# Kernel tuning notes

Measured on AMD Instinct MI355X. Metric: run time of the kernel, lower is better.

Reference implementation:

```python
import jax, jax.numpy as jnp
import numpy as np
from math import sqrt

N = 8192
INPUT_SIZE = 256
D_MODEL = 256


def setup_inputs() -> dict:
    key = jax.random.key(0)
    k1, k2, k3, k4 = jax.random.split(key, 4)
    x = jax.random.normal(k1, (N, INPUT_SIZE), dtype=jnp.float32)
    adj = jax.random.randint(k2, (N, N), 0, 2, dtype=jnp.int32)
    # torch nn.Linear(input_size, d_model): weight [d_model, input_size], bias [d_model]
    bound = 1.0 / sqrt(INPUT_SIZE)
    Vw = jax.random.uniform(k3, (D_MODEL, INPUT_SIZE), dtype=jnp.float32, minval=-bound, maxval=bound)
    Vb = jax.random.uniform(k4, (D_MODEL,), dtype=jnp.float32, minval=-bound, maxval=bound)
    return {"x": x, "adj": adj, "Vw": Vw, "Vb": Vb}


def reference(x, adj, Vw, Vb):
    # value = V(x)
    value = x @ Vw.T + Vb                                  # [N, d_model]
    # scores = x x^T / sqrt(d_model), masked where adj == 0
    scores = (x @ x.T) * (1.0 / sqrt(D_MODEL))             # [N, N]
    scores = jnp.where(adj == 0, jnp.float32(-1e9), scores)
    p_attn = jax.nn.softmax(scores, axis=-1)               # [N, N]
    Vs = p_attn @ value                                    # [N, d_model]
    return (Vs, p_attn)
```

## Files before the change

### kernel.cpp

```cpp
#include <hip/hip_runtime.h>
#include <hip/hip_bf16.h>


#define NN 8192
#define DD 256

typedef __attribute__((ext_vector_type(8))) short bf16x8;
typedef __attribute__((ext_vector_type(8))) unsigned short u16x8;
typedef __attribute__((ext_vector_type(4))) float f32x4;

__device__ __forceinline__ unsigned short f2bf(float f) {
  unsigned u = __builtin_bit_cast(unsigned, f);
  u += 0x7fffu + ((u >> 16) & 1u);
  return (unsigned short)(u >> 16);
}
__device__ __forceinline__ float bf2f(unsigned short h) {
  unsigned u = ((unsigned)h) << 16;
  return __builtin_bit_cast(float, u);
}
__device__ __forceinline__ unsigned pack2(float a, float b) {
  return (unsigned)f2bf(a) | ((unsigned)f2bf(b) << 16);
}

__global__ void k_prep_x(const float* __restrict__ x, unsigned short* __restrict__ xb) {
  int t = blockIdx.x * 256 + threadIdx.x;
  const float4* s = reinterpret_cast<const float4*>(x) + (size_t)t * 2;
  float4 f0 = s[0], f1 = s[1];
  uint4 o;
  o.x = pack2(f0.x, f0.y); o.y = pack2(f0.z, f0.w);
  o.z = pack2(f1.x, f1.y); o.w = pack2(f1.z, f1.w);
  reinterpret_cast<uint4*>(xb)[t] = o;
}

__global__ __launch_bounds__(256) void k_value(
    const float* __restrict__ Vw, const float* __restrict__ Vb,
    const unsigned short* __restrict__ xb, unsigned short* __restrict__ vT) {
  __shared__ unsigned short lB[64 * 256];
  int mb = blockIdx.x >> 2, nb = blockIdx.x & 3;
  int tid = threadIdx.x, lane = tid & 63, w = tid >> 6;
  int mw = w >> 1, nw = w & 1;
  {
    int n_l = tid >> 2, q = tid & 3;
#pragma unroll
    for (int o = 0; o < 8; ++o) {
      int k0 = q * 64 + o * 8;
      const float4* src = reinterpret_cast<const float4*>(Vw + (nb * 64 + n_l) * DD + k0);
      float4 g0 = src[0], g1 = src[1];
      uint4 pk;
      pk.x = pack2(g0.x, g0.y); pk.y = pack2(g0.z, g0.w);
      pk.z = pack2(g1.x, g1.y); pk.w = pack2(g1.z, g1.w);
      *reinterpret_cast<uint4*>(reinterpret_cast<char*>(lB) + n_l * 512 + ((k0 * 2) ^ ((n_l & 7) << 4))) = pk;
    }
  }
  bf16x8 aR[2][8];
#pragma unroll
  for (int mf = 0; mf < 2; ++mf) {
    int rg = mb * 64 + mw * 32 + mf * 16 + (lane & 15);
    const char* base = reinterpret_cast<const char*>(xb + (size_t)rg * DD);
#pragma unroll
    for (int ks = 0; ks < 8; ++ks)
      aR[mf][ks] = *reinterpret_cast<const bf16x8*>(base + ks * 64 + ((lane >> 4) * 16));
  }
  __syncthreads();
  f32x4 acc[2][2] = {};
#pragma unroll
  for (int ks = 0; ks < 8; ++ks) {
    int kb = ks * 64 + ((lane >> 4) * 16);
#pragma unroll
    for (int nf = 0; nf < 2; ++nf) {
      int n = nw * 32 + nf * 16 + (lane & 15);
      bf16x8 b = *reinterpret_cast<const bf16x8*>(reinterpret_cast<const char*>(lB) + n * 512 + (kb ^ ((n & 7) << 4)));
#pragma unroll
      for (int mf = 0; mf < 2; ++mf)
        acc[mf][nf] = __builtin_amdgcn_mfma_f32_16x16x32_bf16(aR[mf][ks], b, acc[mf][nf], 0, 0, 0);
    }
  }
#pragma unroll
  for (int nf = 0; nf < 2; ++nf) {
    int n_g = nb * 64 + nw * 32 + nf * 16 + (lane & 15);
    float vb = Vb[n_g];
#pragma unroll
    for (int mf = 0; mf < 2; ++mf) {
      int m_g = mb * 64 + mw * 32 + mf * 16 + ((lane >> 4) << 2);
      ushort4 h;
      h.x = f2bf(acc[mf][nf][0] + vb);
      h.y = f2bf(acc[mf][nf][1] + vb);
      h.z = f2bf(acc[mf][nf][2] + vb);
      h.w = f2bf(acc[mf][nf][3] + vb);
      *reinterpret_cast<ushort4*>(vT + (size_t)n_g * NN + m_g) = h;
    }
  }
}

__global__ __launch_bounds__(256) void k_pass1(
    const unsigned short* __restrict__ xb, const int* __restrict__ adj,
    unsigned short* __restrict__ ews, float* __restrict__ lpart) {
  __shared__ char smem[65536];
  int rb = blockIdx.x >> 6, cb = blockIdx.x & 63;
  int tid = threadIdx.x, lane = tid & 63, w = tid >> 6;
  int mw = w >> 1, wc = w & 1;
#pragma unroll
  for (int c = 0; c < 16; ++c) {
    int id = c * 256 + tid;
    int col = id >> 5, oct = id & 31;
    uint4 v = *reinterpret_cast<const uint4*>(xb + (size_t)(cb * 128 + col) * DD + oct * 8);
    *reinterpret_cast<uint4*>(smem + col * 512 + ((oct * 16) ^ ((col & 7) << 4))) = v;
  }
  bf16x8 aR[2][8];
#pragma unroll
  for (int mf = 0; mf < 2; ++mf) {
    int rg = rb * 64 + mw * 32 + mf * 16 + (lane & 15);
    const char* base = reinterpret_cast<const char*>(xb + (size_t)rg * DD);
#pragma unroll
    for (int ks = 0; ks < 8; ++ks)
      aR[mf][ks] = *reinterpret_cast<const bf16x8*>(base + ks * 64 + ((lane >> 4) * 16));
  }
  __syncthreads();
  int r0 = rb * 64 + mw * 32 + ((lane >> 4) << 2);
  int c0 = cb * 128 + wc * 64 + (lane & 15);
  int aj[2][4][4];
#pragma unroll
  for (int mf = 0; mf < 2; ++mf)
#pragma unroll
    for (int nf = 0; nf < 4; ++nf)
#pragma unroll
      for (int i = 0; i < 4; ++i)
        aj[mf][nf][i] = __builtin_nontemporal_load(adj + (size_t)(r0 + mf * 16 + i) * NN + (c0 + nf * 16));
  f32x4 acc[2][4] = {};
#pragma unroll
  for (int ks = 0; ks < 8; ++ks) {
    int kb = ks * 64 + ((lane >> 4) * 16);
#pragma unroll
    for (int nf = 0; nf < 4; ++nf) {
      int cc = wc * 64 + nf * 16 + (lane & 15);
      bf16x8 b = *reinterpret_cast<const bf16x8*>(smem + cc * 512 + (kb ^ ((cc & 7) << 4)));
#pragma unroll
      for (int mf = 0; mf < 2; ++mf)
        acc[mf][nf] = __builtin_amdgcn_mfma_f32_16x16x32_bf16(aR[mf][ks], b, acc[mf][nf], 0, 0, 0);
    }
  }
#pragma unroll
  for (int mf = 0; mf < 2; ++mf)
#pragma unroll
    for (int nf = 0; nf < 4; ++nf)
#pragma unroll
      for (int i = 0; i < 4; ++i) {
        float e = aj[mf][nf][i] ? __expf(acc[mf][nf][i] * 0.0625f) : 0.f;
        unsigned short h = f2bf(e);
        ews[(size_t)(r0 + mf * 16 + i) * NN + (c0 + nf * 16)] = h;
        acc[mf][nf][i] = bf2f(h);
      }
  __syncthreads();
  float* ls = reinterpret_cast<float*>(smem);
#pragma unroll
  for (int mf = 0; mf < 2; ++mf)
#pragma unroll
    for (int i = 0; i < 4; ++i) {
      float r = acc[mf][0][i] + acc[mf][1][i] + acc[mf][2][i] + acc[mf][3][i];
      r += __shfl_xor(r, 1); r += __shfl_xor(r, 2);
      r += __shfl_xor(r, 4); r += __shfl_xor(r, 8);
      if ((lane & 15) == 0)
        ls[wc * 64 + mw * 32 + mf * 16 + ((lane >> 4) << 2) + i] = r;
    }
  __syncthreads();
  if (tid < 64)
    lpart[(size_t)cb * NN + rb * 64 + tid] = ls[tid] + ls[64 + tid];
}

__global__ void k_reduce_l(const float* __restrict__ lpart, float* __restrict__ rl) {
  int i = blockIdx.x * 256 + threadIdx.x;
  float s = 0.f;
  for (int c = 0; c < 64; ++c) s += lpart[(size_t)c * NN + i];
  rl[i] = s > 0.f ? 1.f / s : 0.f;
}

__global__ __launch_bounds__(512) void k_vs(
    const unsigned short* __restrict__ ews, const unsigned short* __restrict__ vT,
    const float* __restrict__ rl, unsigned short* __restrict__ vspb) {
  __shared__ char lV[2][65536];
  int rt = blockIdx.x >> 2, ck = blockIdx.x & 3;
  int tid = threadIdx.x, lane = tid & 63, w = tid >> 6;
  int ln = lane & 15, kq = lane >> 4;
  int row = rt * 128 + w * 16 + ln;
  const unsigned short* ap = ews + (size_t)row * NN + ck * 2048 + kq * 8;

#define LOADB(G, KC)                                                                     \
  _Pragma("unroll") for (int q = 0; q < 8; ++q) {                                        \
    int id_ = q * 512 + tid, n_ = id_ >> 4, o_ = id_ & 15;                               \
    (G)[q] = *reinterpret_cast<const uint4*>(vT + (size_t)n_ * NN + ck * 2048 + (KC) * 128 + o_ * 8); \
  }
#define DSWRITE(G, BB)                                                                   \
  _Pragma("unroll") for (int q = 0; q < 8; ++q) {                                        \
    int id_ = q * 512 + tid, n_ = id_ >> 4, o_ = id_ & 15;                               \
    *reinterpret_cast<uint4*>(&lV[BB][n_ * 256 + ((o_ * 16) ^ ((n_ & 7) << 4))]) = (G)[q]; \
  }
#define LOADA(A, KC)                                                                     \
  _Pragma("unroll") for (int s_ = 0; s_ < 4; ++s_)                                       \
    (A)[s_] = *reinterpret_cast<const bf16x8*>(ap + (KC) * 128 + s_ * 32);

  uint4 gB[8];
  bf16x8 aC[4], aN[4];
  LOADB(gB, 0);
  LOADA(aC, 0);
  DSWRITE(gB, 0);
  __syncthreads();

  f32x4 acc[16] = {};
  for (int kc = 0; kc < 16; ++kc) {
    bool has = kc < 15;
    if (has) {
      LOADB(gB, kc + 1);
      LOADA(aN, kc + 1);
    }
    const char* bufc = lV[kc & 1];
#pragma unroll
    for (int ks = 0; ks < 4; ++ks) {
#pragma unroll
      for (int nf = 0; nf < 16; ++nf) {
        int n = nf * 16 + ln;
        bf16x8 b = *reinterpret_cast<const bf16x8*>(bufc + n * 256 + ((ks * 64 + kq * 16) ^ ((n & 7) << 4)));
        acc[nf] = __builtin_amdgcn_mfma_f32_16x16x32_bf16(aC[ks], b, acc[nf], 0, 0, 0);
      }
    }
    if (has) DSWRITE(gB, (kc + 1) & 1);
    __syncthreads();
#pragma unroll
    for (int s = 0; s < 4; ++s) aC[s] = aN[s];
  }

  int rowo = rt * 128 + w * 16 + kq * 4;
#pragma unroll
  for (int i = 0; i < 4; ++i) {
    float rli = rl[rowo + i];
#pragma unroll
    for (int nf = 0; nf < 16; ++nf) {
      int n = nf * 16 + ln;
      vspb[((size_t)ck * NN + rowo + i) * DD + n] = f2bf(acc[nf][i] * rli);
    }
  }
#undef LOADB
#undef DSWRITE
#undef LOADA
}

__global__ void k_norm(const unsigned short* __restrict__ ews, const float* __restrict__ rl,
                       float* __restrict__ pout) {
  size_t t = (size_t)blockIdx.x * 256 + threadIdx.x;
  float r = rl[t >> 10];
  u16x8 v = *reinterpret_cast<const u16x8*>(ews + t * 8);
  f32x4 o0, o1;
  o0[0] = bf2f(v[0]) * r; o0[1] = bf2f(v[1]) * r; o0[2] = bf2f(v[2]) * r; o0[3] = bf2f(v[3]) * r;
  o1[0] = bf2f(v[4]) * r; o1[1] = bf2f(v[5]) * r; o1[2] = bf2f(v[6]) * r; o1[3] = bf2f(v[7]) * r;
  f32x4* pd = reinterpret_cast<f32x4*>(pout + t * 8);
  __builtin_nontemporal_store(o0, pd);
  __builtin_nontemporal_store(o1, pd + 1);
}

__global__ void k_reduce_vs(const unsigned short* __restrict__ vspb, float* __restrict__ vout) {
  int t = blockIdx.x * 256 + threadIdx.x;
  float s[8] = {};
#pragma unroll
  for (int c = 0; c < 4; ++c) {
    u16x8 v = *reinterpret_cast<const u16x8*>(vspb + (size_t)c * NN * DD + (size_t)t * 8);
#pragma unroll
    for (int j = 0; j < 8; ++j) s[j] += bf2f(v[j]);
  }
  float4 o0, o1;
  o0.x = s[0]; o0.y = s[1]; o0.z = s[2]; o0.w = s[3];
  o1.x = s[4]; o1.y = s[5]; o1.z = s[6]; o1.w = s[7];
  float4* d = reinterpret_cast<float4*>(vout + (size_t)t * 8);
  d[0] = o0; d[1] = o1;
}

extern "C" void kernel_launch(void* const* d_in, const int* in_sizes, int n_in,
                              void* d_out, int out_size, void* d_ws, size_t ws_size,
                              hipStream_t stream) {
  const float* x   = (const float*)d_in[0];
  const int*   adj = (const int*)d_in[1];
  const float* Vw  = (const float*)d_in[2];
  const float* Vb  = (const float*)d_in[3];
  float* out   = (float*)d_out;
  float* vs_out = out;
  float* p_out  = out + (size_t)NN * DD;
  char* ws = (char*)d_ws;
  unsigned short* xb   = (unsigned short*)(ws);
  unsigned short* vT   = (unsigned short*)(ws + ((size_t)4  << 20));
  float* lpart         = (float*)(ws + ((size_t)8  << 20));
  float* rl            = (float*)(ws + ((size_t)10 << 20));
  unsigned short* vspb = (unsigned short*)(ws + ((size_t)11 << 20));
  unsigned short* ews  = (unsigned short*)(ws + ((size_t)27 << 20));

  k_prep_x<<<dim3(1024), dim3(256), 0, stream>>>(x, xb);
  k_value<<<dim3(512), dim3(256), 0, stream>>>(Vw, Vb, xb, vT);
  k_pass1<<<dim3(8192), dim3(256), 0, stream>>>(xb, adj, ews, lpart);
  k_reduce_l<<<dim3(32), dim3(256), 0, stream>>>(lpart, rl);
  k_vs<<<dim3(256), dim3(512), 0, stream>>>(ews, vT, rl, vspb);
  k_norm<<<dim3(32768), dim3(256), 0, stream>>>(ews, rl, p_out);
  k_reduce_vs<<<dim3(1024), dim3(256), 0, stream>>>(vspb, vs_out);
}
```

Measured before the change: 325.8 us.

## Pack adjacency mask into bits in a separate pass and add nontemporal loads

Adds a prepass that reads the int32 adjacency matrix with coalesced nontemporal vector loads and packs it into a bitmask. k_pass1 then reads one 64-bit mask word per row instead of scattered strided int32 loads. The nontemporal ews loads in k_vs and k_norm are meant to keep these streams from polluting cache. The same 256MB of adj is still read once, so the gain rests on better coalescing in pass1, at the cost of an extra kernel launch and an 8MB write.

```diff
diff --git a/kernel.cpp b/kernel.cpp
--- a/kernel.cpp
+++ b/kernel.cpp
@@ -8,6 +8,7 @@
 typedef __attribute__((ext_vector_type(8))) short bf16x8;
 typedef __attribute__((ext_vector_type(8))) unsigned short u16x8;
 typedef __attribute__((ext_vector_type(4))) float f32x4;
+typedef __attribute__((ext_vector_type(4))) int i32x4;
 
 __device__ __forceinline__ unsigned short f2bf(float f) {
   unsigned u = __builtin_bit_cast(unsigned, f);
@@ -30,6 +31,19 @@
   o.x = pack2(f0.x, f0.y); o.y = pack2(f0.z, f0.w);
   o.z = pack2(f1.x, f1.y); o.w = pack2(f1.z, f1.w);
   reinterpret_cast<uint4*>(xb)[t] = o;
+}
+
+__global__ void k_prep_adj(const int* __restrict__ adj, unsigned char* __restrict__ adjp) {
+  size_t t = (size_t)blockIdx.x * 256 + threadIdx.x;
+  const i32x4* s = reinterpret_cast<const i32x4*>(adj) + t * 2;
+  i32x4 v0 = __builtin_nontemporal_load(s);
+  i32x4 v1 = __builtin_nontemporal_load(s + 1);
+  unsigned b = 0;
+  b |= (v0[0] != 0) ? 1u : 0u;  b |= (v0[1] != 0) ? 2u : 0u;
+  b |= (v0[2] != 0) ? 4u : 0u;  b |= (v0[3] != 0) ? 8u : 0u;
+  b |= (v1[0] != 0) ? 16u : 0u; b |= (v1[1] != 0) ? 32u : 0u;
+  b |= (v1[2] != 0) ? 64u : 0u; b |= (v1[3] != 0) ? 128u : 0u;
+  adjp[t] = (unsigned char)b;
 }
 
 __global__ __launch_bounds__(256) void k_value(
@@ -93,12 +107,13 @@
 }
 
 __global__ __launch_bounds__(256) void k_pass1(
-    const unsigned short* __restrict__ xb, const int* __restrict__ adj,
+    const unsigned short* __restrict__ xb, const unsigned long long* __restrict__ adjp,
     unsigned short* __restrict__ ews, float* __restrict__ lpart) {
   __shared__ char smem[65536];
   int rb = blockIdx.x >> 6, cb = blockIdx.x & 63;
   int tid = threadIdx.x, lane = tid & 63, w = tid >> 6;
   int mw = w >> 1, wc = w & 1;
+  int ln = lane & 15, kq = lane >> 4;
 #pragma unroll
   for (int c = 0; c < 16; ++c) {
     int id = c * 256 + tid;
@@ -109,43 +124,42 @@
   bf16x8 aR[2][8];
 #pragma unroll
   for (int mf = 0; mf < 2; ++mf) {
-    int rg = rb * 64 + mw * 32 + mf * 16 + (lane & 15);
+    int rg = rb * 64 + mw * 32 + mf * 16 + ln;
     const char* base = reinterpret_cast<const char*>(xb + (size_t)rg * DD);
 #pragma unroll
     for (int ks = 0; ks < 8; ++ks)
-      aR[mf][ks] = *reinterpret_cast<const bf16x8*>(base + ks * 64 + ((lane >> 4) * 16));
-  }
-  __syncthreads();
-  int r0 = rb * 64 + mw * 32 + ((lane >> 4) << 2);
-  int c0 = cb * 128 + wc * 64 + (lane & 15);
-  int aj[2][4][4];
+      aR[mf][ks] = *reinterpret_cast<const bf16x8*>(base + ks * 64 + kq * 16);
+  }
+  __syncthreads();
+  int r0 = rb * 64 + mw * 32 + (kq << 2);
+  unsigned long long mrow[2][4];
 #pragma unroll
   for (int mf = 0; mf < 2; ++mf)
 #pragma unroll
-    for (int nf = 0; nf < 4; ++nf)
-#pragma unroll
-      for (int i = 0; i < 4; ++i)
-        aj[mf][nf][i] = __builtin_nontemporal_load(adj + (size_t)(r0 + mf * 16 + i) * NN + (c0 + nf * 16));
+    for (int i = 0; i < 4; ++i)
+      mrow[mf][i] = adjp[(size_t)(r0 + mf * 16 + i) * 128 + cb * 2 + wc];
   f32x4 acc[2][4] = {};
 #pragma unroll
   for (int ks = 0; ks < 8; ++ks) {
-    int kb = ks * 64 + ((lane >> 4) * 16);
+    int kb = ks * 64 + kq * 16;
 #pragma unroll
     for (int nf = 0; nf < 4; ++nf) {
-      int cc = wc * 64 + nf * 16 + (lane & 15);
+      int cc = wc * 64 + nf * 16 + ln;
       bf16x8 b = *reinterpret_cast<const bf16x8*>(smem + cc * 512 + (kb ^ ((cc & 7) << 4)));
 #pragma unroll
       for (int mf = 0; mf < 2; ++mf)
         acc[mf][nf] = __builtin_amdgcn_mfma_f32_16x16x32_bf16(aR[mf][ks], b, acc[mf][nf], 0, 0, 0);
     }
   }
+  int c0 = cb * 128 + wc * 64 + ln;
 #pragma unroll
   for (int mf = 0; mf < 2; ++mf)
 #pragma unroll
     for (int nf = 0; nf < 4; ++nf)
 #pragma unroll
       for (int i = 0; i < 4; ++i) {
-        float e = aj[mf][nf][i] ? __expf(acc[mf][nf][i] * 0.0625f) : 0.f;
+        bool on = (mrow[mf][i] >> (nf * 16 + ln)) & 1;
+        float e = on ? __expf(acc[mf][nf][i] * 0.0625f) : 0.f;
         unsigned short h = f2bf(e);
         ews[(size_t)(r0 + mf * 16 + i) * NN + (c0 + nf * 16)] = h;
         acc[mf][nf][i] = bf2f(h);
@@ -159,8 +173,8 @@
       float r = acc[mf][0][i] + acc[mf][1][i] + acc[mf][2][i] + acc[mf][3][i];
       r += __shfl_xor(r, 1); r += __shfl_xor(r, 2);
       r += __shfl_xor(r, 4); r += __shfl_xor(r, 8);
-      if ((lane & 15) == 0)
-        ls[wc * 64 + mw * 32 + mf * 16 + ((lane >> 4) << 2) + i] = r;
+      if (ln == 0)
+        ls[wc * 64 + mw * 32 + mf * 16 + (kq << 2) + i] = r;
     }
   __syncthreads();
   if (tid < 64)
@@ -196,7 +210,7 @@
   }
 #define LOADA(A, KC)                                                                     \
   _Pragma("unroll") for (int s_ = 0; s_ < 4; ++s_)                                       \
-    (A)[s_] = *reinterpret_cast<const bf16x8*>(ap + (KC) * 128 + s_ * 32);
+    (A)[s_] = __builtin_nontemporal_load(reinterpret_cast<const bf16x8*>(ap + (KC) * 128 + s_ * 32));
 
   uint4 gB[8];
   bf16x8 aC[4], aN[4];
@@ -247,7 +261,7 @@
                        float* __restrict__ pout) {
   size_t t = (size_t)blockIdx.x * 256 + threadIdx.x;
   float r = rl[t >> 10];
-  u16x8 v = *reinterpret_cast<const u16x8*>(ews + t * 8);
+  u16x8 v = __builtin_nontemporal_load(reinterpret_cast<const u16x8*>(ews + t * 8));
   f32x4 o0, o1;
   o0[0] = bf2f(v[0]) * r; o0[1] = bf2f(v[1]) * r; o0[2] = bf2f(v[2]) * r; o0[3] = bf2f(v[3]) * r;
   o1[0] = bf2f(v[4]) * r; o1[1] = bf2f(v[5]) * r; o1[2] = bf2f(v[6]) * r; o1[3] = bf2f(v[7]) * r;
@@ -285,14 +299,16 @@
   char* ws = (char*)d_ws;
   unsigned short* xb   = (unsigned short*)(ws);
   unsigned short* vT   = (unsigned short*)(ws + ((size_t)4  << 20));
-  float* lpart         = (float*)(ws + ((size_t)8  << 20));
-  float* rl            = (float*)(ws + ((size_t)10 << 20));
+  float* rl            = (float*)(ws + ((size_t)8  << 20));
+  float* lpart         = (float*)(ws + ((size_t)9  << 20));
   unsigned short* vspb = (unsigned short*)(ws + ((size_t)11 << 20));
   unsigned short* ews  = (unsigned short*)(ws + ((size_t)27 << 20));
+  unsigned char* adjp  = (unsigned char*)(ws + ((size_t)156 << 20));
 
   k_prep_x<<<dim3(1024), dim3(256), 0, stream>>>(x, xb);
+  k_prep_adj<<<dim3(32768), dim3(256), 0, stream>>>(adj, adjp);
   k_value<<<dim3(512), dim3(256), 0, stream>>>(Vw, Vb, xb, vT);
-  k_pass1<<<dim3(8192), dim3(256), 0, stream>>>(xb, adj, ews, lpart);
+  k_pass1<<<dim3(8192), dim3(256), 0, stream>>>(xb, (const unsigned long long*)adjp, ews, lpart);
   k_reduce_l<<<dim3(32), dim3(256), 0, stream>>>(lpart, rl);
   k_vs<<<dim3(256), dim3(512), 0, stream>>>(ews, vT, rl, vspb);
   k_norm<<<dim3(32768), dim3(256), 0, stream>>>(ews, rl, p_out);
```

Measured after the change: 364.6 us. 1.12x slower.
